# Optimization experiments

Measured on AMD Instinct MI355X. Metric: run time of the kernel, lower is better.

The kernel has to match this reference:

```python
import jax, jax.numpy as jnp
import numpy as np

N = 100000   # nodes
E = 1000000  # edges
DIN = 128    # atom_in_features
DE = 16      # edge_attr_dim
H = 128      # hidden width (preprocess/cheb/postprocess)
K = 3        # Chebyshev order
EPS = 1e-5


def setup_inputs() -> dict:
    key = jax.random.key(0)
    ks = jax.random.split(key, 16)
    s = 0.02
    return {
        "x": jax.random.normal(ks[0], (N, DIN), jnp.float32),
        "edge_index": jax.random.randint(ks[1], (2, E), 0, N),
        "edge_attr": jax.random.normal(ks[2], (E, DE), jnp.float32),
        # AtomEdgeInteraction linear: (DIN+DE) -> H
        "w_int": jax.random.normal(ks[3], (DIN + DE, H), jnp.float32) * s,
        "b_int": jnp.zeros((H,), jnp.float32),
        # preprocess layer 1: Linear + BatchNorm + ReLU
        "w_pre": jax.random.normal(ks[4], (H, H), jnp.float32) * s,
        "b_pre": jnp.zeros((H,), jnp.float32),
        "g_pre": jnp.ones((H,), jnp.float32),
        "be_pre": jnp.zeros((H,), jnp.float32),
        # ChebConv layers: weight [K, in, out] + bias
        "cheb1_w": jax.random.normal(ks[5], (K, H, H), jnp.float32) * s,
        "cheb1_b": jnp.zeros((H,), jnp.float32),
        "cheb2_w": jax.random.normal(ks[6], (K, H, H), jnp.float32) * s,
        "cheb2_b": jnp.zeros((H,), jnp.float32),
        # postprocess: Linear + BatchNorm + ReLU
        "w_post": jax.random.normal(ks[7], (H, H), jnp.float32) * s,
        "b_post": jnp.zeros((H,), jnp.float32),
        "g_post": jnp.ones((H,), jnp.float32),
        "be_post": jnp.zeros((H,), jnp.float32),
        # output layer H -> 1
        "w_out": jax.random.normal(ks[8], (H, 1), jnp.float32) * s,
        "b_out": jnp.zeros((1,), jnp.float32),
    }


def _bn(z, g, b):
    # BatchNorm1d, training-mode batch statistics (biased variance, like torch)
    m = z.mean(0)
    v = ((z - m) ** 2).mean(0)
    return g * (z - m) * jax.lax.rsqrt(v + EPS) + b


def _cheb(h, W, b, row, col, norm):
    # ChebConv with sym normalization, lambda_max=2 => L_hat = -D^{-1/2} A D^{-1/2}
    def lhat(z):
        return jax.ops.segment_sum(norm[:, None] * z[row], col, num_segments=N)

    Tx0 = h
    out = Tx0 @ W[0]
    Tx1 = lhat(Tx0)
    out = out + Tx1 @ W[1]
    for k in range(2, W.shape[0]):
        Tx2 = 2.0 * lhat(Tx1) - Tx0
        out = out + Tx2 @ W[k]
        Tx0, Tx1 = Tx1, Tx2
    return out + b


def reference(x, edge_index, edge_attr,
              w_int, b_int,
              w_pre, b_pre, g_pre, be_pre,
              cheb1_w, cheb1_b, cheb2_w, cheb2_b,
              w_post, b_post, g_post, be_post,
              w_out, b_out):
    row, col = edge_index[0], edge_index[1]
    ones_e = jnp.ones((E,), x.dtype)

    # AtomEdgeInteraction: gather -> concat -> linear -> scatter_mean over col
    comb = jnp.concatenate([x[row], edge_attr], axis=-1)  # [E, DIN+DE]
    upd = comb @ w_int + b_int                             # [E, H]
    cnt = jax.ops.segment_sum(ones_e, col, num_segments=N)
    h = jax.ops.segment_sum(upd, col, num_segments=N) / jnp.clip(cnt, 1.0)[:, None]

    # preprocess layer 1 (Linear + BN + ReLU; dropout rate 0)
    h = jax.nn.relu(_bn(h @ w_pre + b_pre, g_pre, be_pre))

    # sym-normalized edge coefficients for scaled Laplacian
    deg = jax.ops.segment_sum(ones_e, row, num_segments=N)
    dis = jnp.where(deg > 0, jax.lax.rsqrt(jnp.maximum(deg, 1.0)), 0.0)
    norm = -dis[row] * dis[col]  # [E]

    h = jax.nn.relu(_cheb(h, cheb1_w, cheb1_b, row, col, norm))
    h = jax.nn.relu(_cheb(h, cheb2_w, cheb2_b, row, col, norm))

    # postprocess (Linear + BN + ReLU)
    h = jax.nn.relu(_bn(h @ w_post + b_post, g_post, be_post))

    # output layer, squeeze(-1) -> [N]
    return (h @ w_out + b_out).squeeze(-1)
```

## Files before the change

kernel.cpp:

```cpp
#include <hip/hip_runtime.h>
#include <hip/hip_bf16.h>

using u16 = unsigned short;
using u32 = unsigned int;

#define NN 100000
#define NE 1000000
#define NBKT 196
#define NBLK 489

typedef __attribute__((ext_vector_type(8))) short bfrag;
typedef __attribute__((ext_vector_type(4))) float ffrag;

#define BF16ONE2 0x3F803F80u

__device__ __forceinline__ float bf2f(u16 u) { return __uint_as_float(((u32)u) << 16); }
__device__ __forceinline__ u16 f2bf(float f) {
  u32 x = __float_as_uint(f);
  return (u16)((x + 0x7fffu + ((x >> 16) & 1u)) >> 16);
}
__device__ __forceinline__ float rdv(const void* p, long i, int f) {
  return f ? bf2f(((const u16*)p)[i]) : ((const float*)p)[i];
}
__device__ __forceinline__ void acc8(float* a, uint4 v, float w) {
// ... 154 lines not shown

__global__ void k_scat(const int* __restrict__ ei, const int* __restrict__ bofs,
                       const int* __restrict__ rbofs, const int* __restrict__ bbase,
                       const int* __restrict__ rbbase, u32* __restrict__ sle,
                       u32* __restrict__ srow, u16* __restrict__ srl) {
  __shared__ int cc[NBKT], cr[NBKT], cbase[NBKT], rbase[NBKT];
  int t = threadIdx.x, blk = blockIdx.x;
  for (int i = t; i < NBKT; i += 256) {
    cc[i] = 0;
    cr[i] = 0;
    cbase[i] = bbase[i] + bofs[i * NBLK + blk];
    rbase[i] = rbbase[i] + rbofs[i * NBLK + blk];
  }
  __syncthreads();
  long base = (long)blk * 2048;
#pragma unroll
  for (int i = 0; i < 8; i++) {
    long e = base + i * 256 + t;
    if (e < NE) {
      int c = ei[NE + e], r = ei[e];
      int k1 = atomicAdd(&cc[c >> 9], 1);
      int d1 = cbase[c >> 9] + k1;
      sle[d1] = ((u32)(c & 511) << 20) | (u32)e;
      srow[d1] = (u32)r;
      int k2 = atomicAdd(&cr[r >> 9], 1);
      int d2 = rbase[r >> 9] + k2;
      srl[d2] = (u16)(r & 511);
    }
  }
}

__global__ void k_fine(const u32* __restrict__ sle, const u32* __restrict__ srow,
                       const int* __restrict__ bbase, int* __restrict__ off,
                       int2* __restrict__ cpk) {
  __shared__ u32 hist[512];
  __shared__ u32 ss[256];
  int t = threadIdx.x, b = blockIdx.x;
  hist[t] = 0;
  hist[t + 256] = 0;
  __syncthreads();
  int lo = bbase[b], hi = bbase[b + 1];
  for (int p = lo + t; p < hi; p += 256) atomicAdd(&hist[sle[p] >> 20], 1);
  __syncthreads();
  u32 a = hist[2 * t], bb = hist[2 * t + 1];
  ss[t] = a + bb;
  __syncthreads();
  for (int st = 1; st < 256; st <<= 1) {
    u32 x = (t >= st) ? ss[t - st] : 0;
    __syncthreads();
    ss[t] += x;
    __syncthreads();
  }
  u32 base = ss[t] - a - bb;
  u32 c0 = (u32)lo + base, c1 = (u32)lo + base + a;
  hist[2 * t] = c0;
  hist[2 * t + 1] = c1;
  int col0 = b * 512 + 2 * t, col1 = col0 + 1;
  if (col0 < NN) off[col0] = (int)c0;
  if (col1 < NN) off[col1] = (int)c1;
  __syncthreads();
  for (int p = lo + t; p < hi; p += 256) {
    u32 v = sle[p];
    u32 pos = atomicAdd(&hist[v >> 20], 1);
    cpk[pos] = make_int2((int)srow[p], (int)(v & 0xFFFFFu));
  }
}

__global__ void k_deg(const u16* __restrict__ srl, const int* __restrict__ rbbase,
                      int* __restrict__ deg) {
  __shared__ int hist[512];
  int t = threadIdx.x, b = blockIdx.x;
  hist[t] = 0;
  hist[t + 256] = 0;
  __syncthreads();
  int lo = rbbase[b], hi = rbbase[b + 1];
  for (int p = lo + t; p < hi; p += 256) atomicAdd(&hist[srl[p]], 1);
  __syncthreads();
  int n0 = b * 512 + t, n1 = n0 + 256;
  if (n0 < NN) deg[n0] = hist[t];
  if (n1 < NN) deg[n1] = hist[t + 256];
}

template <int BN>
__global__ __launch_bounds__(256) void k_spmm(const u16* __restrict__ src,
                                              u16* __restrict__ dst,
                                              const int* __restrict__ off,
                                              const int2* __restrict__ cpk,
                                              const float* __restrict__ cnorm,
                                              const float* __restrict__ ab) {
  int t = threadIdx.x;
  int node = blockIdx.x * 8 + (t >> 5);
  if (node >= NN) return;
  int l = t & 31;
  int half = l >> 4;
  int c = (l & 15) * 8;
  float A[8], Bb[8];
  if (BN) {
#pragma unroll
    for (int j = 0; j < 8; j++) {
      A[j] = ab[c + j];
      Bb[j] = ab[128 + c + j];
    }
  }
  int p0 = off[node], p1 = off[node + 1];
  float a[8];
#pragma unroll
  for (int j = 0; j < 8; j++) a[j] = 0.f;
  const u16* sp = src + c;
  for (int p = p0 + half; p < p1; p += 8) {
    int rr[4];
    float w[4];
#pragma unroll
    for (int u = 0; u < 4; u++) {
      int q = p + u * 2;
      int qc = q < p1 ? q : p1 - 1;
      rr[u] = cpk[qc].x;
      w[u] = (q < p1) ? cnorm[qc] : 0.f;
    }
#pragma unroll
    for (int u = 0; u < 4; u++) {
      uint4 v = *(const uint4*)(sp + (long)rr[u] * 128);
      if (BN) acc8bn(a, v, w[u], A, Bb);
      else acc8(a, v, w[u]);
    }
  }
#pragma unroll
  for (int j = 0; j < 8; j++) a[j] += __shfl_xor(a[j], 16);
  if (half) return;
  uint4 o;
  o.x = (u32)f2bf(a[0]) | ((u32)f2bf(a[1]) << 16);
  o.y = (u32)f2bf(a[2]) | ((u32)f2bf(a[3]) << 16);
  o.z = (u32)f2bf(a[4]) | ((u32)f2bf(a[5]) << 16);
  o.w = (u32)f2bf(a[6]) | ((u32)f2bf(a[7]) << 16);
  *(uint4*)(dst + (long)node * 128 + c) = o;
}

template <int WEIGHTED>
__device__ __forceinline__ void gather_lds(u16* sA, const u16* __restrict__ src,
                                           const int* __restrict__ off,
                                           const int2* __restrict__ cpk,
                                           const float* __restrict__ cnorm, int r0) {
  int tid = threadIdx.x;
  int grp = tid >> 4;
  int c = (tid & 15) * 8;
  const u16* sp = src + c;
#pragma unroll
  for (int i = 0; i < 4; i++) {
    int nl = grp * 4 + i;
    int node = r0 + nl;
    float a[8];
#pragma unroll
    for (int j = 0; j < 8; j++) a[j] = 0.f;
    if (node < NN) {
      int p0 = off[node], p1 = off[node + 1];
      for (int p = p0; p < p1; p += 8) {
        int rr[8];
        float w[8];
#pragma unroll
        for (int u = 0; u < 8; u++) {
          int q = p + u;
          int qc = q < p1 ? q : p1 - 1;
          rr[u] = cpk[qc].x;
          w[u] = (q < p1) ? (WEIGHTED ? cnorm[qc] : 1.f) : 0.f;
        }
#pragma unroll
        for (int u = 0; u < 8; u++)
          acc8(a, *(const uint4*)(sp + (long)rr[u] * 128), w[u]);
      }
    }
    uint4 o;
    o.x = (u32)f2bf(a[0]) | ((u32)f2bf(a[1]) << 16);
    o.y = (u32)f2bf(a[2]) | ((u32)f2bf(a[3]) << 16);
    o.z = (u32)f2bf(a[4]) | ((u32)f2bf(a[5]) << 16);
    o.w = (u32)f2bf(a[6]) | ((u32)f2bf(a[7]) << 16);
    *(uint4*)(sA + nl * ASTRIDE + c) = o;
  }
}

__global__ __launch_bounds__(256) void k_asum(const void* __restrict__ eattr,
                                              const u32* __restrict__ gp,
                                              u16* __restrict__ asum,
                                              const int* __restrict__ off,
                                              const int2* __restrict__ cpk,
                                              const int* __restrict__ deg,
                                              float* __restrict__ cnorm) {
  int t = blockIdx.x * 256 + threadIdx.x;
  int node = t >> 4;
  if (node >= NN) return;
  int j = t & 15;
  int p0 = off[node], p1 = off[node + 1];
  int dn = deg[node];
  float ndis = dn > 0 ? -rsqrtf((float)dn) : 0.f;
  for (int p = p0 + j; p < p1; p += 16)
    cnorm[p] = ndis * rsqrtf((float)deg[cpk[p].x]);
  float a = 0.f;
  if (gp[0] == BF16ONE2) {
    const u16* e16 = (const u16*)eattr;
    for (int p = p0; p < p1; p += 8) {
      float s[8];
#pragma unroll
      for (int u = 0; u < 8; u++) {
        int q = p + u;
        int qc = q < p1 ? q : p1 - 1;
        float v = bf2f(e16[(long)cpk[qc].y * 16 + j]);
        s[u] = (q < p1) ? v : 0.f;
      }
      a += ((s[0] + s[1]) + (s[2] + s[3])) + ((s[4] + s[5]) + (s[6] + s[7]));
    }
  } else {
    const float* e32 = (const float*)eattr;
    for (int p = p0; p < p1; p += 8) {
      float s[8];
#pragma unroll
      for (int u = 0; u < 8; u++) {
        int q = p + u;
        int qc = q < p1 ? q : p1 - 1;
        float v = e32[(long)cpk[qc].y * 16 + j];
        s[u] = (q < p1) ? v : 0.f;
      }
      a += ((s[0] + s[1]) + (s[2] + s[3])) + ((s[4] + s[5]) + (s[6] + s[7]));
    }
  }
  asum[(long)node * 16 + j] = f2bf(a);
}

struct MArgs {
  const void* A0; const u16* W0T; int a0raw;
  const float* bias;
  u16* out;
  const u32* gp;
  float* part;
};

__global__ __launch_bounds__(256) void k_mgemm(MArgs m) {
  constexpr int ROWS = 128, RT = 8, TPR = 2, SEGW = 64;
  __shared__ __align__(16) u16 sA[ROWS * ASTRIDE];
  int tid = threadIdx.x;
  int wv = tid >> 6, lane = tid & 63;
  int col16 = lane & 15, quad = lane >> 4;
  int r0 = blockIdx.x * ROWS;

  ffrag acc[RT * 2];
#pragma unroll
  for (int i = 0; i < RT * 2; i++)
#pragma unroll
    for (int g = 0; g < 4; g++) acc[i][g] = 0.f;

  {
    int row = tid / TPR, seg = tid % TPR;
    int ra = r0 + row;
    if (ra >= NN) ra = NN - 1;
    bool f32a = m.a0raw && (m.gp[0] != BF16ONE2);
    if (f32a) {
      const float* gs = (const float*)m.A0 + (long)ra * 128 + seg * SEGW;
      u32* lp = (u32*)(sA + row * ASTRIDE + seg * SEGW);
#pragma unroll
// ... 53 lines not shown
      }
    }
  }
  if (m.part) {
    __shared__ float ps[256], pq[256];
    int col = tid & 127, hf = tid >> 7;
    float s = 0.f, q = 0.f;
#pragma unroll
    for (int r = 0; r < 64; r++) {
      int rr = hf * 64 + r;
      if (r0 + rr < NN) {
        float v = bf2f(sA[rr * ESTRIDE + col]);
        s += v;
        q += v * v;
      }
    }
    ps[tid] = s;
    pq[tid] = q;
    __syncthreads();
    if (tid < 128) {
      m.part[(long)blockIdx.x * 256 + tid] = ps[tid] + ps[tid + 128];
      m.part[(long)blockIdx.x * 256 + 128 + tid] = pq[tid] + pq[tid + 128];
    }
  }
}

__global__ __launch_bounds__(256) void k_etpre(const u16* __restrict__ Xg,
                                               const u16* __restrict__ asum,
                                               const u16* __restrict__ Wet,
                                               const u16* __restrict__ Wpre,
                                               const float* __restrict__ b_int,
                                               const float* __restrict__ b_pre,
                                               const int* __restrict__ off,
                                               const int2* __restrict__ cpk,
                                               u16* __restrict__ out, float* part) {
  __shared__ __align__(16) u16 sA[64 * ASTRIDE];
  __shared__ __align__(16) u16 sE[64 * 32];
  int tid = threadIdx.x;
  int wv = tid >> 6, lane = tid & 63;
  int col16 = lane & 15, quad = lane >> 4;
  int r0 = blockIdx.x * 64;

  gather_lds<0>(sA, Xg, off, cpk, nullptr, r0);
  {
    int row = tid >> 2, seg = tid & 3;
    int ra = r0 + row;
    if (ra >= NN) ra = NN - 1;
    if (seg < 2)
      *(uint4*)(sE + row * 32 + seg * 8) = *(const uint4*)(asum + (long)ra * 16 + seg * 8);
    else
      *(uint4*)(sE + row * 32 + seg * 8) = make_uint4(0, 0, 0, 0);
  }
  bfrag be[2];
#pragma unroll
  for (int c = 0; c < 2; c++)
    be[c] = *(const bfrag*)(Wet + (long)(wv * 32 + c * 16 + col16) * 32 + quad * 8);
  __syncthreads();
  ffrag accE[8];
#pragma unroll
  for (int i = 0; i < 8; i++)
#pragma unroll
    for (int g = 0; g < 4; g++) accE[i][g] = 0.f;
#pragma unroll
  for (int rt = 0; rt < 4; rt++) {
    bfrag af = *(const bfrag*)(sE + (rt * 16 + col16) * 32 + quad * 8);
    accE[rt * 2 + 0] = __builtin_amdgcn_mfma_f32_16x16x32_bf16(af, be[0], accE[rt * 2 + 0], 0, 0, 0);
    accE[rt * 2 + 1] = __builtin_amdgcn_mfma_f32_16x16x32_bf16(af, be[1], accE[rt * 2 + 1], 0, 0, 0);
  }
#pragma unroll
  for (int rt = 0; rt < 4; rt++)
#pragma unroll
    for (int g = 0; g < 4; g++) {
      int rr = rt * 16 + quad * 4 + g;
      int r = r0 + rr;
      int cc = (r < NN) ? off[r + 1] - off[r] : 0;
      float inv = 1.f / (float)(cc > 1 ? cc : 1);
// ... 13 lines not shown
    for (int kb = 0; kb < 4; kb++)
      b1[c][kb] = *(const bfrag*)(Wpre + (long)(wv * 32 + c * 16 + col16) * 128 + kb * 32 + quad * 8);
  __syncthreads();
  ffrag a2[8];
#pragma unroll
  for (int i = 0; i < 8; i++)
#pragma unroll
    for (int g = 0; g < 4; g++) a2[i][g] = 0.f;
#pragma unroll
  for (int kb = 0; kb < 4; kb++)
#pragma unroll
    for (int rt = 0; rt < 4; rt++) {
      bfrag af = *(const bfrag*)(sA + (rt * 16 + col16) * ASTRIDE + kb * 32 + quad * 8);
      a2[rt * 2 + 0] = __builtin_amdgcn_mfma_f32_16x16x32_bf16(af, b1[0][kb], a2[rt * 2 + 0], 0, 0, 0);
      a2[rt * 2 + 1] = __builtin_amdgcn_mfma_f32_16x16x32_bf16(af, b1[1][kb], a2[rt * 2 + 1], 0, 0, 0);
    }
  __syncthreads();
#pragma unroll
  for (int rt = 0; rt < 4; rt++)
#pragma unroll
    for (int c = 0; c < 2; c++) {
      int col = wv * 32 + c * 16 + col16;
      float bj = b_pre[col];
#pragma unroll
      for (int g = 0; g < 4; g++)
        sA[(rt * 16 + quad * 4 + g) * ESTRIDE + col] = f2bf(a2[rt * 2 + c][g] + bj);
    }
  __syncthreads();
  {
    int rr = tid >> 2, d = tid & 3;
    int rowg = r0 + rr;
    if (rowg < NN) {
      const u16* sp2 = sA + rr * ESTRIDE + d * 32;
      uint4* o = (uint4*)(out + (long)rowg * 128 + d * 32);
#pragma unroll
      for (int e = 0; e < 4; e++) {
        const uint2* s2 = (const uint2*)(sp2 + e * 8);
        uint2 lo = s2[0], hi = s2[1];
        o[e] = make_uint4(lo.x, lo.y, hi.x, hi.y);
      }
    }
  }
  {
    __shared__ float ps[256], pq[256];
    int col = tid & 127, hf = tid >> 7;
    float s = 0.f, q = 0.f;
#pragma unroll
    for (int r = 0; r < 32; r++) {
      int rr = hf * 32 + r;
      if (r0 + rr < NN) {
        float v = bf2f(sA[rr * ESTRIDE + col]);
        s += v;
        q += v * v;
      }
    }
    ps[tid] = s;
    pq[tid] = q;
    __syncthreads();
    if (tid < 128) {
      part[(long)blockIdx.x * 256 + tid] = ps[tid] + ps[tid + 128];
      part[(long)blockIdx.x * 256 + 128 + tid] = pq[tid] + pq[tid + 128];
    }
  }
}

template <int BN>
__global__ __launch_bounds__(256) void k_cheb(const u16* __restrict__ hb,
                                              const u16* __restrict__ T1,
                                              const int* __restrict__ off,
                                              const int2* __restrict__ cpk,
                                              const float* __restrict__ cnorm,
                                              const u16* __restrict__ WD,
                                              const u16* __restrict__ W1,
                                              const u16* __restrict__ V2,
                                              const float* __restrict__ bias,
                                              const float* __restrict__ ab,
                                              u16* __restrict__ out) {
  __shared__ __align__(16) u16 sA[64 * ASTRIDE];
  int tid = threadIdx.x;
  int wv = tid >> 6, lane = tid & 63;
  int col16 = lane & 15, quad = lane >> 4;
  int r0 = blockIdx.x * 64;

  gather_lds<1>(sA, T1, off, cpk, cnorm, r0);
  bfrag bv[2][4];
#pragma unroll
  for (int c = 0; c < 2; c++)
#pragma unroll
    for (int kb = 0; kb < 4; kb++)
      bv[c][kb] = *(const bfrag*)(V2 + (long)(wv * 32 + c * 16 + col16) * 128 + kb * 32 + quad * 8);
  __syncthreads();
  ffrag acc[8];
#pragma unroll
  for (int i = 0; i < 8; i++)
#pragma unroll
    for (int g = 0; g < 4; g++) acc[i][g] = 0.f;
#pragma unroll
  for (int kb = 0; kb < 4; kb++)
#pragma unroll
    for (int rt = 0; rt < 4; rt++) {
      bfrag af = *(const bfrag*)(sA + (rt * 16 + col16) * ASTRIDE + kb * 32 + quad * 8);
      acc[rt * 2 + 0] = __builtin_amdgcn_mfma_f32_16x16x32_bf16(af, bv[0][kb], acc[rt * 2 + 0], 0, 0, 0);
      acc[rt * 2 + 1] = __builtin_amdgcn_mfma_f32_16x16x32_bf16(af, bv[1][kb], acc[rt * 2 + 1], 0, 0, 0);
    }
  __syncthreads();

  {
    int row = tid >> 2, seg = tid & 3;
    int ra = r0 + row;
    if (ra >= NN) ra = NN - 1;
    const u16* gs = hb + (long)ra * 128 + seg * 32;
    uint4* lp = (uint4*)(sA + row * ASTRIDE + seg * 32);
    if (BN) {
#pragma unroll
      for (int e = 0; e < 4; e++) {
        uint4 v = *(const uint4*)(gs + e * 8);
        int cb = seg * 32 + e * 8;
        float f0 = fmaxf(fmaf(ab[cb + 0], __uint_as_float(v.x << 16), ab[128 + cb + 0]), 0.f);
        float f1 = fmaxf(fmaf(ab[cb + 1], __uint_as_float(v.x & 0xffff0000u), ab[128 + cb + 1]), 0.f);
        float f2 = fmaxf(fmaf(ab[cb + 2], __uint_as_float(v.y << 16), ab[128 + cb + 2]), 0.f);
        float f3 = fmaxf(fmaf(ab[cb + 3], __uint_as_float(v.y & 0xffff0000u), ab[128 + cb + 3]), 0.f);
        float f4 = fmaxf(fmaf(ab[cb + 4], __uint_as_float(v.z << 16), ab[128 + cb + 4]), 0.f);
        float f5 = fmaxf(fmaf(ab[cb + 5], __uint_as_float(v.z & 0xffff0000u), ab[128 + cb + 5]), 0.f);
        float f6 = fmaxf(fmaf(ab[cb + 6], __uint_as_float(v.w << 16), ab[128 + cb + 6]), 0.f);
        float f7 = fmaxf(fmaf(ab[cb + 7], __uint_as_float(v.w & 0xffff0000u), ab[128 + cb + 7]), 0.f);
        uint4 o;
        o.x = (u32)f2bf(f0) | ((u32)f2bf(f1) << 16);
        o.y = (u32)f2bf(f2) | ((u32)f2bf(f3) << 16);
        o.z = (u32)f2bf(f4) | ((u32)f2bf(f5) << 16);
        o.w = (u32)f2bf(f6) | ((u32)f2bf(f7) << 16);
        lp[e] = o;
      }
    } else {
#pragma unroll
      for (int e = 0; e < 4; e++) lp[e] = *(const uint4*)(gs + e * 8);
    }
  }
#pragma unroll
  for (int c = 0; c < 2; c++)
#pragma unroll
    for (int kb = 0; kb < 4; kb++)
      bv[c][kb] = *(const bfrag*)(WD + (long)(wv * 32 + c * 16 + col16) * 128 + kb * 32 + quad * 8);
  __syncthreads();
#pragma unroll
  for (int kb = 0; kb < 4; kb++)
#pragma unroll
    for (int rt = 0; rt < 4; rt++) {
      bfrag af = *(const bfrag*)(sA + (rt * 16 + col16) * ASTRIDE + kb * 32 + quad * 8);
      acc[rt * 2 + 0] = __builtin_amdgcn_mfma_f32_16x16x32_bf16(af, bv[0][kb], acc[rt * 2 + 0], 0, 0, 0);
      acc[rt * 2 + 1] = __builtin_amdgcn_mfma_f32_16x16x32_bf16(af, bv[1][kb], acc[rt * 2 + 1], 0, 0, 0);
    }
  __syncthreads();

  {
    int row = tid >> 2, seg = tid & 3;
    int ra = r0 + row;
    if (ra >= NN) ra = NN - 1;
    const u16* gs = T1 + (long)ra * 128 + seg * 32;
    uint4* lp = (uint4*)(sA + row * ASTRIDE + seg * 32);
#pragma unroll
    for (int e = 0; e < 4; e++) lp[e] = *(const uint4*)(gs + e * 8);
  }
#pragma unroll
  for (int c = 0; c < 2; c++)
#pragma unroll
    for (int kb = 0; kb < 4; kb++)
      bv[c][kb] = *(const bfrag*)(W1 + (long)(wv * 32 + c * 16 + col16) * 128 + kb * 32 + quad * 8);
  __syncthreads();
#pragma unroll
  for (int kb = 0; kb < 4; kb++)
#pragma unroll
    for (int rt = 0; rt < 4; rt++) {
      bfrag af = *(const bfrag*)(sA + (rt * 16 + col16) * ASTRIDE + kb * 32 + quad * 8);
      acc[rt * 2 + 0] = __builtin_amdgcn_mfma_f32_16x16x32_bf16(af, bv[0][kb], acc[rt * 2 + 0], 0, 0, 0);
      acc[rt * 2 + 1] = __builtin_amdgcn_mfma_f32_16x16x32_bf16(af, bv[1][kb], acc[rt * 2 + 1], 0, 0, 0);
    }
  __syncthreads();

#pragma unroll
  for (int rt = 0; rt < 4; rt++)
#pragma unroll
// ... 65 lines not shown
    s += h * wout[c];
  }
#pragma unroll
  for (int o = 32; o > 0; o >>= 1) s += __shfl_down(s, o);
  if (lane == 0) {
    float r = s + bout[0];
    if (gp[0] == BF16ONE2) ((u16*)y)[node] = f2bf(r);
    else ((float*)y)[node] = r;
  }
}

extern "C" void kernel_launch(void* const* d_in, const int* in_sizes, int n_in,
                              void* d_out, int out_size, void* d_ws, size_t ws_size,
                              hipStream_t stream) {
  const void* x = d_in[0];
  const int* ei = (const int*)d_in[1];
  const void* eattr = d_in[2];
  const u32* gp = (const u32*)d_in[7];
  (void)in_sizes; (void)n_in; (void)out_size; (void)ws_size;

  char* w = (char*)d_ws;
  size_t p = 0;
  auto alloc = [&](size_t b) { size_t r = p; p += (b + 255) & ~(size_t)255; return r; };
  size_t o_deg = alloc((size_t)NN * 4);
  size_t o_off = alloc((size_t)(NN + 1) * 4);
  size_t o_bcnt = alloc((size_t)NBKT * NBLK * 4);
  size_t o_rbcnt = alloc((size_t)NBKT * NBLK * 4);
  size_t o_btot = alloc((size_t)2 * NBKT * 4);
  size_t o_bbase = alloc((size_t)(NBKT + 1) * 4);
  size_t o_rbbase = alloc((size_t)(NBKT + 1) * 4);
  size_t o_ab = alloc(512 * 4);
  size_t o_wq = alloc((size_t)151552 * 2);
  size_t o_wf = alloc((size_t)1281 * 4);
  size_t o_cpk = alloc((size_t)NE * 8);
  size_t o_cnrm = alloc((size_t)NE * 4);
  size_t o_asum = alloc((size_t)NN * 16 * 2);
  size_t o_part = alloc((size_t)1563 * 256 * 4);
  size_t o_Bx = alloc((size_t)NN * 128 * 2);
  size_t o_Bt = alloc((size_t)NN * 128 * 2);

  int* deg = (int*)(w + o_deg);
  int* off = (int*)(w + o_off);
  int* bcnt = (int*)(w + o_bcnt);
  int* rbcnt = (int*)(w + o_rbcnt);
  int* btot = (int*)(w + o_btot);
  int* bbase = (int*)(w + o_bbase);
  int* rbbase = (int*)(w + o_rbbase);
  float* abA = (float*)(w + o_ab);
  float* abB = abA + 256;
  u16* wq = (u16*)(w + o_wq);
  float* wf = (float*)(w + o_wf);
  int2* cpk = (int2*)(w + o_cpk);
  float* cnrm = (float*)(w + o_cnrm);
  u16* asum = (u16*)(w + o_asum);
  float* part = (float*)(w + o_part);
  u16* Bx = (u16*)(w + o_Bx);
  u16* Bt = (u16*)(w + o_Bt);
  u32* sle = (u32*)Bx;
  u32* srow = sle + NE;
  u16* srl = (u16*)(srow + NE);

  int gS = (NN + 7) / 8;
  int gG1 = (NN + 127) / 128;
  int gG2 = (NN + 63) / 64;

  {
    PrepArgs a;
    for (int i = 0; i < 16; i++) a.in[i] = d_in[3 + i];
    k_prep<<<64, 256, 0, stream>>>(a, gp, wq, wf);
  }

  k_cnt<<<NBLK, 256, 0, stream>>>(ei, bcnt, rbcnt);
  k_bscan<<<2 * NBKT, 256, 0, stream>>>(bcnt, rbcnt, btot);
  k_bbase<<<1, 256, 0, stream>>>(btot, bbase, rbbase, off);
  k_scat<<<NBLK, 256, 0, stream>>>(ei, bcnt, rbcnt, bbase, rbbase, sle, srow, srl);
  k_fine<<<NBKT, 256, 0, stream>>>(sle, srow, bbase, off, cpk);
  k_deg<<<NBKT, 256, 0, stream>>>(srl, rbbase, deg);

  k_asum<<<(NN * 16 + 255) / 256, 256, 0, stream>>>(eattr, gp, asum, off, cpk, deg, cnrm);

  {
    MArgs a = {};
    a.A0 = x; a.W0T = wq + OWXT; a.a0raw = 1;
    a.out = Bx; a.gp = gp;
    k_mgemm<<<gG1, 256, 0, stream>>>(a);
  }
  k_etpre<<<gG2, 256, 0, stream>>>(Bx, asum, wq + OWET, wq + OWPRE, wf + 0, wf + 128,
                                   off, cpk, Bt, part);
  k_redfin<<<8, 256, 0, stream>>>(part, wf + 256, wf + 384, abA, gG2);

  k_spmm<1><<<gS, 256, 0, stream>>>(Bt, Bx, off, cpk, cnrm, abA);
  k_cheb<1><<<gG2, 256, 0, stream>>>(Bt, Bx, off, cpk, cnrm,
                                     wq + OWD1, wq + OW11, wq + OV21, wf + 512, abA, Bt);

  k_spmm<0><<<gS, 256, 0, stream>>>(Bt, Bx, off, cpk, cnrm, nullptr);
  k_cheb<0><<<gG2, 256, 0, stream>>>(Bt, Bx, off, cpk, cnrm,
                                     wq + OWD2, wq + OW12, wq + OV22, wf + 640, nullptr, Bt);

  {
    MArgs a = {};
    a.A0 = Bt; a.W0T = wq + OWPOST;
    a.bias = wf + 768; a.out = Bx; a.gp = gp; a.part = part;
    k_mgemm<<<gG1, 256, 0, stream>>>(a);
  }
  k_redfin<<<8, 256, 0, stream>>>(part, wf + 896, wf + 1024, abB, gG1);
  k_out<<<(NN + 3) / 4, 256, 0, stream>>>(Bx, abB, wf + 1152, wf + 1280, gp, d_out);
}
```

Baseline: 671.1 us.

## Split packed CSR into row array and pre-scatter edge attributes into CSR order

The packed (row, edge-id) CSR array is replaced by a plain row-index array plus an edge-to-position map. A new kernel uses that map to scatter edge attributes, converted to bf16, into CSR order, so the per-node edge-attribute sum reads contiguous memory instead of random rows. This halves the index bytes the SpMM and gather kernels read. k_cheb also gets a second LDS tile so the gathered and dense operands load before a single barrier. The cost is an extra 32 MB scatter pass, buffer aliasing (Bt shares storage with eac, pose shares with cnorm) and more LDS per block, which may lower occupancy.

```diff
diff --git a/kernel.cpp b/kernel.cpp
--- a/kernel.cpp
+++ b/kernel.cpp
@@ -210,7 +210,7 @@
 
 __global__ void k_fine(const u32* __restrict__ sle, const u32* __restrict__ srow,
                        const int* __restrict__ bbase, int* __restrict__ off,
-                       int2* __restrict__ cpk) {
+                       int* __restrict__ crow, int* __restrict__ pose) {
   __shared__ u32 hist[512];
   __shared__ u32 ss[256];
   int t = threadIdx.x, b = blockIdx.x;
@@ -240,7 +240,8 @@
   for (int p = lo + t; p < hi; p += 256) {
     u32 v = sle[p];
     u32 pos = atomicAdd(&hist[v >> 20], 1);
-    cpk[pos] = make_int2((int)srow[p], (int)(v & 0xFFFFFu));
+    crow[pos] = (int)srow[p];
+    pose[v & 0xFFFFFu] = (int)pos;
   }
 }
 
@@ -259,11 +260,46 @@
   if (n1 < NN) deg[n1] = hist[t + 256];
 }
 
+__global__ void k_escat(const void* __restrict__ eattr, const u32* __restrict__ gp,
+                        const int* __restrict__ pose, u16* __restrict__ eac) {
+  long t = (long)blockIdx.x * 256 + threadIdx.x;
+  long e0 = t * 4;
+  if (e0 >= NE) return;
+  int n = (e0 + 4 <= NE) ? 4 : (int)(NE - e0);
+  if (gp[0] == BF16ONE2) {
+    const uint4* src = (const uint4*)((const u16*)eattr + e0 * 16);
+    for (int i = 0; i < n; i++) {
+      long pos = pose[e0 + i];
+      uint4* d = (uint4*)(eac + pos * 16);
+      d[0] = src[i * 2];
+      d[1] = src[i * 2 + 1];
+    }
+  } else {
+    const float* src = (const float*)eattr + e0 * 16;
+    for (int i = 0; i < n; i++) {
+      long pos = pose[e0 + i];
+      uint4* d = (uint4*)(eac + pos * 16);
+      uint4 o0, o1;
+      const float* s = src + i * 16;
+      o0.x = (u32)f2bf(s[0]) | ((u32)f2bf(s[1]) << 16);
+      o0.y = (u32)f2bf(s[2]) | ((u32)f2bf(s[3]) << 16);
+      o0.z = (u32)f2bf(s[4]) | ((u32)f2bf(s[5]) << 16);
+      o0.w = (u32)f2bf(s[6]) | ((u32)f2bf(s[7]) << 16);
+      o1.x = (u32)f2bf(s[8]) | ((u32)f2bf(s[9]) << 16);
+      o1.y = (u32)f2bf(s[10]) | ((u32)f2bf(s[11]) << 16);
+      o1.z = (u32)f2bf(s[12]) | ((u32)f2bf(s[13]) << 16);
+      o1.w = (u32)f2bf(s[14]) | ((u32)f2bf(s[15]) << 16);
+      d[0] = o0;
+      d[1] = o1;
+    }
+  }
+}
+
 template <int BN>
 __global__ __launch_bounds__(256) void k_spmm(const u16* __restrict__ src,
                                               u16* __restrict__ dst,
                                               const int* __restrict__ off,
-                                              const int2* __restrict__ cpk,
+                                              const int* __restrict__ crow,
                                               const float* __restrict__ cnorm,
                                               const float* __restrict__ ab) {
   int t = threadIdx.x;
@@ -292,7 +328,7 @@
     for (int u = 0; u < 4; u++) {
       int q = p + u * 2;
       int qc = q < p1 ? q : p1 - 1;
-      rr[u] = cpk[qc].x;
+      rr[u] = crow[qc];
       w[u] = (q < p1) ? cnorm[qc] : 0.f;
     }
 #pragma unroll
@@ -316,7 +352,7 @@
 template <int WEIGHTED>
 __device__ __forceinline__ void gather_lds(u16* sA, const u16* __restrict__ src,
                                            const int* __restrict__ off,
-                                           const int2* __restrict__ cpk,
+                                           const int* __restrict__ crow,
                                            const float* __restrict__ cnorm, int r0) {
   int tid = threadIdx.x;
   int grp = tid >> 4;
@@ -338,7 +374,7 @@
         for (int u = 0; u < 8; u++) {
           int q = p + u;
           int qc = q < p1 ? q : p1 - 1;
-          rr[u] = cpk[qc].x;
+          rr[u] = crow[qc];
           w[u] = (q < p1) ? (WEIGHTED ? cnorm[qc] : 1.f) : 0.f;
         }
 #pragma unroll
@@ -355,11 +391,10 @@
   }
 }
 
-__global__ __launch_bounds__(256) void k_asum(const void* __restrict__ eattr,
-                                              const u32* __restrict__ gp,
+__global__ __launch_bounds__(256) void k_asum(const u16* __restrict__ eac,
                                               u16* __restrict__ asum,
                                               const int* __restrict__ off,
-                                              const int2* __restrict__ cpk,
+                                              const int* __restrict__ crow,
                                               const int* __restrict__ deg,
                                               float* __restrict__ cnorm) {
   int t = blockIdx.x * 256 + threadIdx.x;
@@ -370,36 +405,17 @@
   int dn = deg[node];
   float ndis = dn > 0 ? -rsqrtf((float)dn) : 0.f;
   for (int p = p0 + j; p < p1; p += 16)
-    cnorm[p] = ndis * rsqrtf((float)deg[cpk[p].x]);
-  float a = 0.f;
-  if (gp[0] == BF16ONE2) {
-    const u16* e16 = (const u16*)eattr;
-    for (int p = p0; p < p1; p += 8) {
-      float s[8];
-#pragma unroll
-      for (int u = 0; u < 8; u++) {
-        int q = p + u;
-        int qc = q < p1 ? q : p1 - 1;
-        float v = bf2f(e16[(long)cpk[qc].y * 16 + j]);
-        s[u] = (q < p1) ? v : 0.f;
-      }
-      a += ((s[0] + s[1]) + (s[2] + s[3])) + ((s[4] + s[5]) + (s[6] + s[7]));
-    }
-  } else {
-    const float* e32 = (const float*)eattr;
-    for (int p = p0; p < p1; p += 8) {
-      float s[8];
-#pragma unroll
-      for (int u = 0; u < 8; u++) {
-        int q = p + u;
-        int qc = q < p1 ? q : p1 - 1;
-        float v = e32[(long)cpk[qc].y * 16 + j];
-        s[u] = (q < p1) ? v : 0.f;
-      }
-      a += ((s[0] + s[1]) + (s[2] + s[3])) + ((s[4] + s[5]) + (s[6] + s[7]));
-    }
-  }
-  asum[(long)node * 16 + j] = f2bf(a);
+    cnorm[p] = ndis * rsqrtf((float)deg[crow[p]]);
+  float a0 = 0.f, a1 = 0.f, a2 = 0.f, a3 = 0.f;
+  int p = p0;
+  for (; p + 4 <= p1; p += 4) {
+    a0 += bf2f(eac[(long)p * 16 + j]);
+    a1 += bf2f(eac[(long)(p + 1) * 16 + j]);
+    a2 += bf2f(eac[(long)(p + 2) * 16 + j]);
+    a3 += bf2f(eac[(long)(p + 3) * 16 + j]);
+  }
+  for (; p < p1; p++) a0 += bf2f(eac[(long)p * 16 + j]);
+  asum[(long)node * 16 + j] = f2bf((a0 + a1) + (a2 + a3));
 }
 
 struct MArgs {
@@ -519,7 +535,7 @@
                                                const float* __restrict__ b_int,
                                                const float* __restrict__ b_pre,
                                                const int* __restrict__ off,
-                                               const int2* __restrict__ cpk,
+                                               const int* __restrict__ crow,
                                                u16* __restrict__ out, float* part) {
   __shared__ __align__(16) u16 sA[64 * ASTRIDE];
   __shared__ __align__(16) u16 sE[64 * 32];
@@ -528,7 +544,7 @@
   int col16 = lane & 15, quad = lane >> 4;
   int r0 = blockIdx.x * 64;
 
-  gather_lds<0>(sA, Xg, off, cpk, nullptr, r0);
+  gather_lds<0>(sA, Xg, off, crow, nullptr, r0);
   {
     int row = tid >> 2, seg = tid & 3;
     int ra = r0 + row;
@@ -644,7 +660,7 @@
 __global__ __launch_bounds__(256) void k_cheb(const u16* __restrict__ hb,
                                               const u16* __restrict__ T1,
                                               const int* __restrict__ off,
-                                              const int2* __restrict__ cpk,
+                                              const int* __restrict__ crow,
                                               const float* __restrict__ cnorm,
                                               const u16* __restrict__ WD,
                                               const u16* __restrict__ W1,
@@ -653,40 +669,19 @@
                                               const float* __restrict__ ab,
                                               u16* __restrict__ out) {
   __shared__ __align__(16) u16 sA[64 * ASTRIDE];
+  __shared__ __align__(16) u16 sB[64 * ASTRIDE];
   int tid = threadIdx.x;
   int wv = tid >> 6, lane = tid & 63;
   int col16 = lane & 15, quad = lane >> 4;
   int r0 = blockIdx.x * 64;
 
-  gather_lds<1>(sA, T1, off, cpk, cnorm, r0);
-  bfrag bv[2][4];
-#pragma unroll
-  for (int c = 0; c < 2; c++)
-#pragma unroll
-    for (int kb = 0; kb < 4; kb++)
-      bv[c][kb] = *(const bfrag*)(V2 + (long)(wv * 32 + c * 16 + col16) * 128 + kb * 32 + quad * 8);
-  __syncthreads();
-  ffrag acc[8];
-#pragma unroll
-  for (int i = 0; i < 8; i++)
-#pragma unroll
-    for (int g = 0; g < 4; g++) acc[i][g] = 0.f;
-#pragma unroll
-  for (int kb = 0; kb < 4; kb++)
-#pragma unroll
-    for (int rt = 0; rt < 4; rt++) {
-      bfrag af = *(const bfrag*)(sA + (rt * 16 + col16) * ASTRIDE + kb * 32 + quad * 8);
-      acc[rt * 2 + 0] = __builtin_amdgcn_mfma_f32_16x16x32_bf16(af, bv[0][kb], acc[rt * 2 + 0], 0, 0, 0);
-      acc[rt * 2 + 1] = __builtin_amdgcn_mfma_f32_16x16x32_bf16(af, bv[1][kb], acc[rt * 2 + 1], 0, 0, 0);
-    }
-  __syncthreads();
-
+  gather_lds<1>(sA, T1, off, crow, cnorm, r0);
   {
     int row = tid >> 2, seg = tid & 3;
     int ra = r0 + row;
     if (ra >= NN) ra = NN - 1;
     const u16* gs = hb + (long)ra * 128 + seg * 32;
-    uint4* lp = (uint4*)(sA + row * ASTRIDE + seg * 32);
+    uint4* lp = (uint4*)(sB + row * ASTRIDE + seg * 32);
     if (BN) {
 #pragma unroll
       for (int e = 0; e < 4; e++) {
@@ -712,17 +707,36 @@
       for (int e = 0; e < 4; e++) lp[e] = *(const uint4*)(gs + e * 8);
     }
   }
+  bfrag bv[2][4];
+#pragma unroll
+  for (int c = 0; c < 2; c++)
+#pragma unroll
+    for (int kb = 0; kb < 4; kb++)
+      bv[c][kb] = *(const bfrag*)(V2 + (long)(wv * 32 + c * 16 + col16) * 128 + kb * 32 + quad * 8);
+  __syncthreads();
+  ffrag acc[8];
+#pragma unroll
+  for (int i = 0; i < 8; i++)
+#pragma unroll
+    for (int g = 0; g < 4; g++) acc[i][g] = 0.f;
+#pragma unroll
+  for (int kb = 0; kb < 4; kb++)
+#pragma unroll
+    for (int rt = 0; rt < 4; rt++) {
+      bfrag af = *(const bfrag*)(sA + (rt * 16 + col16) * ASTRIDE + kb * 32 + quad * 8);
+      acc[rt * 2 + 0] = __builtin_amdgcn_mfma_f32_16x16x32_bf16(af, bv[0][kb], acc[rt * 2 + 0], 0, 0, 0);
+      acc[rt * 2 + 1] = __builtin_amdgcn_mfma_f32_16x16x32_bf16(af, bv[1][kb], acc[rt * 2 + 1], 0, 0, 0);
+    }
 #pragma unroll
   for (int c = 0; c < 2; c++)
 #pragma unroll
     for (int kb = 0; kb < 4; kb++)
       bv[c][kb] = *(const bfrag*)(WD + (long)(wv * 32 + c * 16 + col16) * 128 + kb * 32 + quad * 8);
-  __syncthreads();
 #pragma unroll
   for (int kb = 0; kb < 4; kb++)
 #pragma unroll
     for (int rt = 0; rt < 4; rt++) {
-      bfrag af = *(const bfrag*)(sA + (rt * 16 + col16) * ASTRIDE + kb * 32 + quad * 8);
+      bfrag af = *(const bfrag*)(sB + (rt * 16 + col16) * ASTRIDE + kb * 32 + quad * 8);
       acc[rt * 2 + 0] = __builtin_amdgcn_mfma_f32_16x16x32_bf16(af, bv[0][kb], acc[rt * 2 + 0], 0, 0, 0);
       acc[rt * 2 + 1] = __builtin_amdgcn_mfma_f32_16x16x32_bf16(af, bv[1][kb], acc[rt * 2 + 1], 0, 0, 0);
     }
@@ -854,12 +868,12 @@
   size_t o_ab = alloc(512 * 4);
   size_t o_wq = alloc((size_t)151552 * 2);
   size_t o_wf = alloc((size_t)1281 * 4);
-  size_t o_cpk = alloc((size_t)NE * 8);
+  size_t o_crow = alloc((size_t)NE * 4);
   size_t o_cnrm = alloc((size_t)NE * 4);
   size_t o_asum = alloc((size_t)NN * 16 * 2);
   size_t o_part = alloc((size_t)1563 * 256 * 4);
   size_t o_Bx = alloc((size_t)NN * 128 * 2);
-  size_t o_Bt = alloc((size_t)NN * 128 * 2);
+  size_t o_eac = alloc((size_t)NE * 16 * 2);
 
   int* deg = (int*)(w + o_deg);
   int* off = (int*)(w + o_off);
@@ -872,17 +886,21 @@
   float* abB = abA + 256;
   u16* wq = (u16*)(w + o_wq);
   float* wf = (float*)(w + o_wf);
-  int2* cpk = (int2*)(w + o_cpk);
+  int* crow = (int*)(w + o_crow);
   float* cnrm = (float*)(w + o_cnrm);
   u16* asum = (u16*)(w + o_asum);
   float* part = (float*)(w + o_part);
   u16* Bx = (u16*)(w + o_Bx);
-  u16* Bt = (u16*)(w + o_Bt);
+  u16* eac = (u16*)(w + o_eac);
+  u16* Bt = eac;
   u32* sle = (u32*)Bx;
   u32* srow = sle + NE;
   u16* srl = (u16*)(srow + NE);
+  int* pose = (int*)cnrm;
 
   int gS = (NN + 7) / 8;
+  int gN16 = (NN * 16 + 255) / 256;
+  int gE4 = (int)((NE / 4 + 255) / 256) + 1;
   int gG1 = (NN + 127) / 128;
   int gG2 = (NN + 63) / 64;
 
@@ -896,10 +914,11 @@
   k_bscan<<<2 * NBKT, 256, 0, stream>>>(bcnt, rbcnt, btot);
   k_bbase<<<1, 256, 0, stream>>>(btot, bbase, rbbase, off);
   k_scat<<<NBLK, 256, 0, stream>>>(ei, bcnt, rbcnt, bbase, rbbase, sle, srow, srl);
-  k_fine<<<NBKT, 256, 0, stream>>>(sle, srow, bbase, off, cpk);
+  k_fine<<<NBKT, 256, 0, stream>>>(sle, srow, bbase, off, crow, pose);
   k_deg<<<NBKT, 256, 0, stream>>>(srl, rbbase, deg);
 
-  k_asum<<<(NN * 16 + 255) / 256, 256, 0, stream>>>(eattr, gp, asum, off, cpk, deg, cnrm);
+  k_escat<<<gE4, 256, 0, stream>>>(eattr, gp, pose, eac);
+  k_asum<<<gN16, 256, 0, stream>>>(eac, asum, off, crow, deg, cnrm);
 
   {
     MArgs a = {};
@@ -908,15 +927,15 @@
     k_mgemm<<<gG1, 256, 0, stream>>>(a);
   }
   k_etpre<<<gG2, 256, 0, stream>>>(Bx, asum, wq + OWET, wq + OWPRE, wf + 0, wf + 128,
-                                   off, cpk, Bt, part);
+                                   off, crow, Bt, part);
   k_redfin<<<8, 256, 0, stream>>>(part, wf + 256, wf + 384, abA, gG2);
 
-  k_spmm<1><<<gS, 256, 0, stream>>>(Bt, Bx, off, cpk, cnrm, abA);
-  k_cheb<1><<<gG2, 256, 0, stream>>>(Bt, Bx, off, cpk, cnrm,
+  k_spmm<1><<<gS, 256, 0, stream>>>(Bt, Bx, off, crow, cnrm, abA);
+  k_cheb<1><<<gG2, 256, 0, stream>>>(Bt, Bx, off, crow, cnrm,
                                      wq + OWD1, wq + OW11, wq + OV21, wf + 512, abA, Bt);
 
-  k_spmm<0><<<gS, 256, 0, stream>>>(Bt, Bx, off, cpk, cnrm, nullptr);
-  k_cheb<0><<<gG2, 256, 0, stream>>>(Bt, Bx, off, cpk, cnrm,
+  k_spmm<0><<<gS, 256, 0, stream>>>(Bt, Bx, off, crow, cnrm, nullptr);
+  k_cheb<0><<<gG2, 256, 0, stream>>>(Bt, Bx, off, crow, cnrm,
                                      wq + OWD2, wq + OW12, wq + OV22, wf + 640, nullptr, Bt);
 
   {
```

Result: slower. 695.2 us (+3.6%).

## Store preprocess output in column-panel layout and gather SpMM panel-by-panel

Applied to the files above, without the earlier changes.

k_etpre now writes its output as 8 panels of 16 columns (panel-major across all nodes), and a new k_spmmP kernel gathers one panel at a time so each pass's random row reads hit a much smaller working set that may stay in cache. The CSR packed int2 array is split into separate row and edge-id arrays, so row-index reads no longer fetch the unused edge id. A third buffer is added so the panel-layout tensor can feed both the first SpMM and the cheb kernel. In exchange the edge list is re-read 8 times per node, and each gather is only 16 bytes wide.

```diff
diff --git a/kernel.cpp b/kernel.cpp
--- a/kernel.cpp
+++ b/kernel.cpp
@@ -210,7 +210,7 @@
 
 __global__ void k_fine(const u32* __restrict__ sle, const u32* __restrict__ srow,
                        const int* __restrict__ bbase, int* __restrict__ off,
-                       int2* __restrict__ cpk) {
+                       int* __restrict__ crow, int* __restrict__ ceid) {
   __shared__ u32 hist[512];
   __shared__ u32 ss[256];
   int t = threadIdx.x, b = blockIdx.x;
@@ -240,7 +240,8 @@
   for (int p = lo + t; p < hi; p += 256) {
     u32 v = sle[p];
     u32 pos = atomicAdd(&hist[v >> 20], 1);
-    cpk[pos] = make_int2((int)srow[p], (int)(v & 0xFFFFFu));
+    crow[pos] = (int)srow[p];
+    ceid[pos] = (int)(v & 0xFFFFFu);
   }
 }
 
@@ -263,7 +264,7 @@
 __global__ __launch_bounds__(256) void k_spmm(const u16* __restrict__ src,
                                               u16* __restrict__ dst,
                                               const int* __restrict__ off,
-                                              const int2* __restrict__ cpk,
+                                              const int* __restrict__ crow,
                                               const float* __restrict__ cnorm,
                                               const float* __restrict__ ab) {
   int t = threadIdx.x;
@@ -292,7 +293,7 @@
     for (int u = 0; u < 4; u++) {
       int q = p + u * 2;
       int qc = q < p1 ? q : p1 - 1;
-      rr[u] = cpk[qc].x;
+      rr[u] = crow[qc];
       w[u] = (q < p1) ? cnorm[qc] : 0.f;
     }
 #pragma unroll
@@ -313,10 +314,70 @@
   *(uint4*)(dst + (long)node * 128 + c) = o;
 }
 
+template <int BN>
+__global__ __launch_bounds__(256) void k_spmmP(const u16* __restrict__ zP,
+                                               u16* __restrict__ dst,
+                                               const int* __restrict__ off,
+                                               const int* __restrict__ crow,
+                                               const float* __restrict__ cnorm,
+                                               const float* __restrict__ ab) {
+  int tid = threadIdx.x;
+  int node = blockIdx.x * 64 + (tid >> 2);
+  bool valid = node < NN;
+  int nc = valid ? node : NN - 1;
+  int s = (tid >> 1) & 1, h = tid & 1;
+  int p0 = off[nc];
+  int p1 = valid ? off[nc + 1] : p0;
+#pragma unroll 1
+  for (int pass = 0; pass < 8; pass++) {
+    const u16* sp = zP + (long)pass * NN * 16 + h * 8;
+    float A[8], Bb[8];
+    if (BN) {
+      int cb = pass * 16 + h * 8;
+#pragma unroll
+      for (int j = 0; j < 8; j++) {
+        A[j] = ab[cb + j];
+        Bb[j] = ab[128 + cb + j];
+      }
+    }
+    float a[8];
+#pragma unroll
+    for (int j = 0; j < 8; j++) a[j] = 0.f;
+    for (int q = p0 + s; q < p1; q += 8) {
+      int rr4[4];
+      float w4[4];
+#pragma unroll
+      for (int u = 0; u < 4; u++) {
+        int qq = q + u * 2;
+        int qc = qq < p1 ? qq : p1 - 1;
+        rr4[u] = crow[qc];
+        w4[u] = (qq < p1) ? cnorm[qc] : 0.f;
+      }
+#pragma unroll
+      for (int u = 0; u < 4; u++) {
+        uint4 v = *(const uint4*)(sp + (long)rr4[u] * 16);
+        if (BN) acc8bn(a, v, w4[u], A, Bb);
+        else acc8(a, v, w4[u]);
+      }
+    }
+#pragma unroll
+    for (int j = 0; j < 8; j++) a[j] += __shfl_xor(a[j], 2);
+    if (!s && valid) {
+      uint4 o;
+      o.x = (u32)f2bf(a[0]) | ((u32)f2bf(a[1]) << 16);
+      o.y = (u32)f2bf(a[2]) | ((u32)f2bf(a[3]) << 16);
+      o.z = (u32)f2bf(a[4]) | ((u32)f2bf(a[5]) << 16);
+      o.w = (u32)f2bf(a[6]) | ((u32)f2bf(a[7]) << 16);
+      *(uint4*)(dst + (long)node * 128 + pass * 16 + h * 8) = o;
+    }
+    __syncthreads();
+  }
+}
+
 template <int WEIGHTED>
 __device__ __forceinline__ void gather_lds(u16* sA, const u16* __restrict__ src,
                                            const int* __restrict__ off,
-                                           const int2* __restrict__ cpk,
+                                           const int* __restrict__ crow,
                                            const float* __restrict__ cnorm, int r0) {
   int tid = threadIdx.x;
   int grp = tid >> 4;
@@ -338,7 +399,7 @@
         for (int u = 0; u < 8; u++) {
           int q = p + u;
           int qc = q < p1 ? q : p1 - 1;
-          rr[u] = cpk[qc].x;
+          rr[u] = crow[qc];
           w[u] = (q < p1) ? (WEIGHTED ? cnorm[qc] : 1.f) : 0.f;
         }
 #pragma unroll
@@ -359,7 +420,8 @@
                                               const u32* __restrict__ gp,
                                               u16* __restrict__ asum,
                                               const int* __restrict__ off,
-                                              const int2* __restrict__ cpk,
+                                              const int* __restrict__ ceid,
+                                              const int* __restrict__ crow,
                                               const int* __restrict__ deg,
                                               float* __restrict__ cnorm) {
   int t = blockIdx.x * 256 + threadIdx.x;
@@ -370,33 +432,33 @@
   int dn = deg[node];
   float ndis = dn > 0 ? -rsqrtf((float)dn) : 0.f;
   for (int p = p0 + j; p < p1; p += 16)
-    cnorm[p] = ndis * rsqrtf((float)deg[cpk[p].x]);
+    cnorm[p] = ndis * rsqrtf((float)deg[crow[p]]);
   float a = 0.f;
   if (gp[0] == BF16ONE2) {
     const u16* e16 = (const u16*)eattr;
     for (int p = p0; p < p1; p += 8) {
-      float s[8];
+      float s8[8];
 #pragma unroll
       for (int u = 0; u < 8; u++) {
         int q = p + u;
         int qc = q < p1 ? q : p1 - 1;
-        float v = bf2f(e16[(long)cpk[qc].y * 16 + j]);
-        s[u] = (q < p1) ? v : 0.f;
-      }
-      a += ((s[0] + s[1]) + (s[2] + s[3])) + ((s[4] + s[5]) + (s[6] + s[7]));
+        float v = bf2f(e16[(long)ceid[qc] * 16 + j]);
+        s8[u] = (q < p1) ? v : 0.f;
+      }
+      a += ((s8[0] + s8[1]) + (s8[2] + s8[3])) + ((s8[4] + s8[5]) + (s8[6] + s8[7]));
     }
   } else {
     const float* e32 = (const float*)eattr;
     for (int p = p0; p < p1; p += 8) {
-      float s[8];
+      float s8[8];
 #pragma unroll
       for (int u = 0; u < 8; u++) {
         int q = p + u;
         int qc = q < p1 ? q : p1 - 1;
-        float v = e32[(long)cpk[qc].y * 16 + j];
-        s[u] = (q < p1) ? v : 0.f;
-      }
-      a += ((s[0] + s[1]) + (s[2] + s[3])) + ((s[4] + s[5]) + (s[6] + s[7]));
+        float v = e32[(long)ceid[qc] * 16 + j];
+        s8[u] = (q < p1) ? v : 0.f;
+      }
+      a += ((s8[0] + s8[1]) + (s8[2] + s8[3])) + ((s8[4] + s8[5]) + (s8[6] + s8[7]));
     }
   }
   asum[(long)node * 16 + j] = f2bf(a);
@@ -519,8 +581,8 @@
                                                const float* __restrict__ b_int,
                                                const float* __restrict__ b_pre,
                                                const int* __restrict__ off,
-                                               const int2* __restrict__ cpk,
-                                               u16* __restrict__ out, float* part) {
+                                               const int* __restrict__ crow,
+                                               u16* __restrict__ outP, float* part) {
   __shared__ __align__(16) u16 sA[64 * ASTRIDE];
   __shared__ __align__(16) u16 sE[64 * 32];
   int tid = threadIdx.x;
@@ -528,7 +590,7 @@
   int col16 = lane & 15, quad = lane >> 4;
   int r0 = blockIdx.x * 64;
 
-  gather_lds<0>(sA, Xg, off, cpk, nullptr, r0);
+  gather_lds<0>(sA, Xg, off, crow, nullptr, r0);
   {
     int row = tid >> 2, seg = tid & 3;
     int ra = r0 + row;
@@ -608,13 +670,20 @@
     int rowg = r0 + rr;
     if (rowg < NN) {
       const u16* sp2 = sA + rr * ESTRIDE + d * 32;
-      uint4* o = (uint4*)(out + (long)rowg * 128 + d * 32);
-#pragma unroll
-      for (int e = 0; e < 4; e++) {
-        const uint2* s2 = (const uint2*)(sp2 + e * 8);
-        uint2 lo = s2[0], hi = s2[1];
-        o[e] = make_uint4(lo.x, lo.y, hi.x, hi.y);
-      }
+      uint2 u0 = ((const uint2*)(sp2 + 0))[0];
+      uint2 u1 = ((const uint2*)(sp2 + 4))[0];
+      uint2 u2 = ((const uint2*)(sp2 + 8))[0];
+      uint2 u3 = ((const uint2*)(sp2 + 12))[0];
+      uint2 u4 = ((const uint2*)(sp2 + 16))[0];
+      uint2 u5 = ((const uint2*)(sp2 + 20))[0];
+      uint2 u6 = ((const uint2*)(sp2 + 24))[0];
+      uint2 u7 = ((const uint2*)(sp2 + 28))[0];
+      uint4* pa = (uint4*)(outP + ((long)(2 * d) * NN + rowg) * 16);
+      uint4* pb = (uint4*)(outP + ((long)(2 * d + 1) * NN + rowg) * 16);
+      pa[0] = make_uint4(u0.x, u0.y, u1.x, u1.y);
+      pa[1] = make_uint4(u2.x, u2.y, u3.x, u3.y);
+      pb[0] = make_uint4(u4.x, u4.y, u5.x, u5.y);
+      pb[1] = make_uint4(u6.x, u6.y, u7.x, u7.y);
     }
   }
   {
@@ -644,7 +713,7 @@
 __global__ __launch_bounds__(256) void k_cheb(const u16* __restrict__ hb,
                                               const u16* __restrict__ T1,
                                               const int* __restrict__ off,
-                                              const int2* __restrict__ cpk,
+                                              const int* __restrict__ crow,
                                               const float* __restrict__ cnorm,
                                               const u16* __restrict__ WD,
                                               const u16* __restrict__ W1,
@@ -658,7 +727,7 @@
   int col16 = lane & 15, quad = lane >> 4;
   int r0 = blockIdx.x * 64;
 
-  gather_lds<1>(sA, T1, off, cpk, cnorm, r0);
+  gather_lds<1>(sA, T1, off, crow, cnorm, r0);
   bfrag bv[2][4];
 #pragma unroll
   for (int c = 0; c < 2; c++)
@@ -685,12 +754,18 @@
     int row = tid >> 2, seg = tid & 3;
     int ra = r0 + row;
     if (ra >= NN) ra = NN - 1;
-    const u16* gs = hb + (long)ra * 128 + seg * 32;
     uint4* lp = (uint4*)(sA + row * ASTRIDE + seg * 32);
     if (BN) {
+      const u16* g0 = hb + ((long)(2 * seg) * NN + ra) * 16;
+      const u16* g1 = hb + ((long)(2 * seg + 1) * NN + ra) * 16;
+      uint4 vv[4];
+      vv[0] = ((const uint4*)g0)[0];
+      vv[1] = ((const uint4*)g0)[1];
+      vv[2] = ((const uint4*)g1)[0];
+      vv[3] = ((const uint4*)g1)[1];
 #pragma unroll
       for (int e = 0; e < 4; e++) {
-        uint4 v = *(const uint4*)(gs + e * 8);
+        uint4 v = vv[e];
         int cb = seg * 32 + e * 8;
         float f0 = fmaxf(fmaf(ab[cb + 0], __uint_as_float(v.x << 16), ab[128 + cb + 0]), 0.f);
         float f1 = fmaxf(fmaf(ab[cb + 1], __uint_as_float(v.x & 0xffff0000u), ab[128 + cb + 1]), 0.f);
@@ -708,6 +783,7 @@
         lp[e] = o;
       }
     } else {
+      const u16* gs = hb + (long)ra * 128 + seg * 32;
 #pragma unroll
       for (int e = 0; e < 4; e++) lp[e] = *(const uint4*)(gs + e * 8);
     }
@@ -854,12 +930,14 @@
   size_t o_ab = alloc(512 * 4);
   size_t o_wq = alloc((size_t)151552 * 2);
   size_t o_wf = alloc((size_t)1281 * 4);
-  size_t o_cpk = alloc((size_t)NE * 8);
+  size_t o_crow = alloc((size_t)NE * 4);
+  size_t o_ceid = alloc((size_t)NE * 4);
   size_t o_cnrm = alloc((size_t)NE * 4);
   size_t o_asum = alloc((size_t)NN * 16 * 2);
   size_t o_part = alloc((size_t)1563 * 256 * 4);
   size_t o_Bx = alloc((size_t)NN * 128 * 2);
   size_t o_Bt = alloc((size_t)NN * 128 * 2);
+  size_t o_Bc = alloc((size_t)NN * 128 * 2);
 
   int* deg = (int*)(w + o_deg);
   int* off = (int*)(w + o_off);
@@ -872,17 +950,20 @@
   float* abB = abA + 256;
   u16* wq = (u16*)(w + o_wq);
   float* wf = (float*)(w + o_wf);
-  int2* cpk = (int2*)(w + o_cpk);
+  int* crow = (int*)(w + o_crow);
+  int* ceid = (int*)(w + o_ceid);
   float* cnrm = (float*)(w + o_cnrm);
   u16* asum = (u16*)(w + o_asum);
   float* part = (float*)(w + o_part);
   u16* Bx = (u16*)(w + o_Bx);
   u16* Bt = (u16*)(w + o_Bt);
-  u32* sle = (u32*)Bx;
+  u16* Bc = (u16*)(w + o_Bc);
+  u32* sle = (u32*)Bc;
   u32* srow = sle + NE;
   u16* srl = (u16*)(srow + NE);
 
   int gS = (NN + 7) / 8;
+  int gN16 = (NN * 16 + 255) / 256;
   int gG1 = (NN + 127) / 128;
   int gG2 = (NN + 63) / 64;
 
@@ -896,10 +977,10 @@
   k_bscan<<<2 * NBKT, 256, 0, stream>>>(bcnt, rbcnt, btot);
   k_bbase<<<1, 256, 0, stream>>>(btot, bbase, rbbase, off);
   k_scat<<<NBLK, 256, 0, stream>>>(ei, bcnt, rbcnt, bbase, rbbase, sle, srow, srl);
-  k_fine<<<NBKT, 256, 0, stream>>>(sle, srow, bbase, off, cpk);
+  k_fine<<<NBKT, 256, 0, stream>>>(sle, srow, bbase, off, crow, ceid);
   k_deg<<<NBKT, 256, 0, stream>>>(srl, rbbase, deg);
 
-  k_asum<<<(NN * 16 + 255) / 256, 256, 0, stream>>>(eattr, gp, asum, off, cpk, deg, cnrm);
+  k_asum<<<gN16, 256, 0, stream>>>(eattr, gp, asum, off, ceid, crow, deg, cnrm);
 
   {
     MArgs a = {};
@@ -908,23 +989,23 @@
     k_mgemm<<<gG1, 256, 0, stream>>>(a);
   }
   k_etpre<<<gG2, 256, 0, stream>>>(Bx, asum, wq + OWET, wq + OWPRE, wf + 0, wf + 128,
-                                   off, cpk, Bt, part);
+                                   off, crow, Bt, part);
   k_redfin<<<8, 256, 0, stream>>>(part, wf + 256, wf + 384, abA, gG2);
 
-  k_spmm<1><<<gS, 256, 0, stream>>>(Bt, Bx, off, cpk, cnrm, abA);
-  k_cheb<1><<<gG2, 256, 0, stream>>>(Bt, Bx, off, cpk, cnrm,
-                                     wq + OWD1, wq + OW11, wq + OV21, wf + 512, abA, Bt);
-
-  k_spmm<0><<<gS, 256, 0, stream>>>(Bt, Bx, off, cpk, cnrm, nullptr);
-  k_cheb<0><<<gG2, 256, 0, stream>>>(Bt, Bx, off, cpk, cnrm,
-                                     wq + OWD2, wq + OW12, wq + OV22, wf + 640, nullptr, Bt);
+  k_spmmP<1><<<gG2, 256, 0, stream>>>(Bt, Bx, off, crow, cnrm, abA);
+  k_cheb<1><<<gG2, 256, 0, stream>>>(Bt, Bx, off, crow, cnrm,
+                                     wq + OWD1, wq + OW11, wq + OV21, wf + 512, abA, Bc);
+
+  k_spmm<0><<<gS, 256, 0, stream>>>(Bc, Bt, off, crow, cnrm, nullptr);
+  k_cheb<0><<<gG2, 256, 0, stream>>>(Bc, Bt, off, crow, cnrm,
+                                     wq + OWD2, wq + OW12, wq + OV22, wf + 640, nullptr, Bc);
 
   {
     MArgs a = {};
-    a.A0 = Bt; a.W0T = wq + OWPOST;
-    a.bias = wf + 768; a.out = Bx; a.gp = gp; a.part = part;
+    a.A0 = Bc; a.W0T = wq + OWPOST;
+    a.bias = wf + 768; a.out = Bt; a.gp = gp; a.part = part;
     k_mgemm<<<gG1, 256, 0, stream>>>(a);
   }
   k_redfin<<<8, 256, 0, stream>>>(part, wf + 896, wf + 1024, abB, gG1);
-  k_out<<<(NN + 3) / 4, 256, 0, stream>>>(Bx, abB, wf + 1152, wf + 1280, gp, d_out);
-}
+  k_out<<<(NN + 3) / 4, 256, 0, stream>>>(Bt, abB, wf + 1152, wf + 1280, gp, d_out);
+}
```

Measured after the change: 746.9 us. +11.3%, slower.
